# Optimization experiments

Hardware: AMD Instinct MI355X
Metric: run time of the kernel (lower is better)

## Reference

```python
import jax, jax.numpy as jnp
import numpy as np
from jax import lax

N, C_IN, C_OUT, H, W, K = 32, 512, 512, 56, 56, 7


def setup_inputs() -> dict:
    key = jax.random.key(0)
    ks = jax.random.split(key, 7)
    s_in = 1.0 / np.sqrt(C_IN)
    s_out = 1.0 / np.sqrt(C_OUT)
    return {
        "x": jax.random.normal(ks[0], (N, C_IN, H, W), dtype=jnp.float32),
        "k": K,
        "w_up": jax.random.normal(ks[1], (C_OUT, C_IN), dtype=jnp.float32) * s_in,
        "b_up": jax.random.normal(ks[2], (C_OUT,), dtype=jnp.float32) * s_in,
        "w_down": jax.random.normal(ks[3], (C_OUT, C_IN), dtype=jnp.float32) * s_in,
        "b_down": jax.random.normal(ks[4], (C_OUT,), dtype=jnp.float32) * s_in,
        "w_final": jax.random.normal(ks[5], (C_OUT, C_OUT), dtype=jnp.float32) * s_out,
        "b_final": jax.random.normal(ks[6], (C_OUT,), dtype=jnp.float32) * s_out,
    }


def _conv1x1(x, w, b):
    # x: [N, Cin, H, W], w: [Cout, Cin] -> [N, Cout, H, W]
    return jnp.einsum("nchw,oc->nohw", x, w) + b[None, :, None, None]


def reference(x, k, w_up, b_up, w_down, b_down, w_final, b_final):
    n, c_in, h, w = x.shape
    c_out = w_up.shape[0]
    pad = (k - 1) // 2

    up = _conv1x1(x, w_up, b_up)  # [N, Cout, H, W]

    # AdaptiveAvgPool2d(k): H, W divisible by k -> exact uniform pooling
    pooled = x.reshape(n, c_in, k, h // k, k, w // k).mean(axis=(3, 5))  # [N, Cin, k, k]
    down = _conv1x1(pooled, w_down, b_down)  # [N, Cout, k, k] dynamic depthwise kernels

    def dw_conv(u, ker):
        # u: [Cout, H, W], ker: [Cout, k, k]; depthwise (groups = Cout)
        return lax.conv_general_dilated(
            u[None],                    # [1, Cout, H, W]
            ker[:, None],               # [Cout, 1, k, k] (OIHW)
            window_strides=(1, 1),
            padding=[(pad, pad), (pad, pad)],
            feature_group_count=c_out,
            dimension_numbers=("NCHW", "OIHW", "NCHW"),
        )[0]

    out = jax.vmap(dw_conv)(up, down)  # [N, Cout, H, W]
    return _conv1x1(out, w_final, b_final)
```

## Files before the change

### kernel.cpp

```cpp
#include <hip/hip_runtime.h>
#include <hip/hip_bf16.h>

typedef unsigned short u16;
typedef _Float16 f16x8 __attribute__((ext_vector_type(8)));
typedef _Float16 f16x4 __attribute__((ext_vector_type(4)));
typedef _Float16 half2v __attribute__((ext_vector_type(2)));
typedef float f32x4 __attribute__((ext_vector_type(4)));
typedef unsigned short ushortx8 __attribute__((ext_vector_type(8)));
typedef unsigned short ushortx4 __attribute__((ext_vector_type(4)));

#define GPTR(p)  ((const __attribute__((address_space(1))) void*)(p))
#define LDSPTR(p) ((__attribute__((address_space(3))) void*)(p))

static __device__ __forceinline__ u16 f2h(float f) {
    _Float16 h = (_Float16)f;
    union { _Float16 h; u16 u; } v; v.h = h; return v.u;
}

__global__ __launch_bounds__(256) void cvtw_kernel(
    const float* __restrict__ wu, const float* __restrict__ wf,
    u16* __restrict__ wub, u16* __restrict__ wfb) {
    int i = blockIdx.x * 256 + threadIdx.x;
    wub[i] = f2h(wu[i]);
    wfb[i] = f2h(wf[i]);
}

__global__ __launch_bounds__(256) void transpose_kernel(
    const float* __restrict__ x, u16* __restrict__ xt) {
    __shared__ float tile[64][65];
    int bid = blockIdx.x;
    int jt = bid % 49;
    int r = bid / 49;
    int ct = r & 7, n = r >> 3;
    const float* src = x + ((size_t)(n * 512 + ct * 64)) * 3136 + jt * 64;
    for (int e = threadIdx.x; e < 1024; e += 256) {
        int i = e >> 4, j4 = (e & 15) * 4;
        float4 v = *(const float4*)(src + (size_t)i * 3136 + j4);
        tile[i][j4]     = v.x;
        tile[i][j4 + 1] = v.y;
        tile[i][j4 + 2] = v.z;
        tile[i][j4 + 3] = v.w;
    }
    __syncthreads();
    u16* dst = xt + ((size_t)(n * 3136 + jt * 64)) * 512 + ct * 64;
    for (int e = threadIdx.x; e < 1024; e += 256) {
        int jj = e >> 4, i4 = (e & 15) * 4;
        ushortx4 o;
        o[0] = f2h(tile[i4][jj]);
        o[1] = f2h(tile[i4 + 1][jj]);
        o[2] = f2h(tile[i4 + 2][jj]);
        o[3] = f2h(tile[i4 + 3][jj]);
        *(ushortx4*)(dst + (size_t)jj * 512 + i4) = o;
    }
}

__global__ __launch_bounds__(128) void poolh_kernel(
    const u16* __restrict__ xt, float* __restrict__ pooled) {
    int bid = blockIdx.x;
    int n = bid / 49, cell = bid - n * 49;
    int py = cell / 7, px = cell - py * 7;
    int t = threadIdx.x;
    float s0 = 0.f, s1 = 0.f, s2 = 0.f, s3 = 0.f;
    const u16* base = xt + ((size_t)(n * 3136 + py * 8 * 56 + px * 8)) * 512 + 4 * t;
    #pragma unroll
    for (int r = 0; r < 8; ++r) {
        #pragma unroll
        for (int cc = 0; cc < 8; ++cc) {
            f16x4 v = *(const f16x4*)(base + (size_t)(r * 56 + cc) * 512);
            s0 += (float)v[0]; s1 += (float)v[1];
            s2 += (float)v[2]; s3 += (float)v[3];
        }
    }
    float* pp = pooled + (size_t)n * 512 * 49 + py * 7 + px;
    pp[(size_t)(4 * t) * 49]     = s0 * (1.f / 64.f);
    pp[(size_t)(4 * t + 1) * 49] = s1 * (1.f / 64.f);
    pp[(size_t)(4 * t + 2) * 49] = s2 * (1.f / 64.f);
    pp[(size_t)(4 * t + 3) * 49] = s3 * (1.f / 64.f);
}

__global__ __launch_bounds__(256) void down_kernel(
    const float* __restrict__ pooled, const float* __restrict__ w_down,
    const float* __restrict__ b_down, float* __restrict__ down) {
    int bid = blockIdx.x;
    int n = bid >> 5, og = bid & 31;
    int wv = threadIdx.x >> 6, lane = threadIdx.x & 63;
    int o0 = og * 16 + wv * 4;
    const float* pp = pooled + (size_t)n * 512 * 49;
    const float* w0 = w_down + (size_t)o0 * 512;
    float a0 = 0, a1 = 0, a2 = 0, a3 = 0;
    int cell = lane < 49 ? lane : 48;
    #pragma unroll 4
    for (int c = 0; c < 512; ++c) {
        float p = pp[c * 49 + cell];
        a0 += p * w0[c];
        a1 += p * w0[512 + c];
        a2 += p * w0[1024 + c];
        a3 += p * w0[1536 + c];
    }
    if (lane < 49) {
        float* dd = down + ((size_t)n * 512 + o0) * 49 + lane;
        dd[0]   = a0 + b_down[o0];
        dd[49]  = a1 + b_down[o0 + 1];
        dd[98]  = a2 + b_down[o0 + 2];
        dd[147] = a3 + b_down[o0 + 3];
    }
}

template <int EPI>
__global__ __launch_bounds__(256) void gemm_kernel(
    const u16* __restrict__ A, const u16* __restrict__ Bt,
    const float* __restrict__ bias, void* __restrict__ Cout) {
    constexpr int K = 512;
    __shared__ u16 As[128 * 32];
    __shared__ u16 Bs[128 * 32];
    int tid = threadIdx.x, wv = tid >> 6, lane = tid & 63;
    int bid = blockIdx.x;
    int tm, tn;
    if (EPI == 0) { tm = (bid >> 5) * 8 + (bid & 7); tn = (bid >> 3) & 3; }
    else          { tn = (bid >> 5) * 8 + (bid & 7); tm = (bid >> 3) & 3; }
    size_t m0 = (size_t)tm * 128, n0 = (size_t)tn * 128;
    int lr = lane & 15, lk = (lane >> 4) * 8;
    int wr = wv >> 1, wc = wv & 1;

    int e0 = wv * 512 + lane * 8;
    int e1 = e0 + 2048;
    const u16* pa0 = A + (m0 + (size_t)(e0 >> 5)) * K + (e0 & 31);
    const u16* pa1 = A + (m0 + (size_t)(e1 >> 5)) * K + (e1 & 31);
    const u16* pb0 = Bt + (n0 + (size_t)(e0 >> 5)) * K + (e0 & 31);
    const u16* pb1 = Bt + (n0 + (size_t)(e1 >> 5)) * K + (e1 & 31);
    u16* sa0 = &As[wv * 512]; u16* sa1 = &As[wv * 512 + 2048];
    u16* sb0 = &Bs[wv * 512]; u16* sb1 = &Bs[wv * 512 + 2048];

    f32x4 acc[4][4] = {};

    for (int kt = 0; kt < K / 32; ++kt) {
        __builtin_amdgcn_global_load_lds(GPTR(pa0), LDSPTR(sa0), 16, 0, 0);
        __builtin_amdgcn_global_load_lds(GPTR(pa1), LDSPTR(sa1), 16, 0, 0);
        __builtin_amdgcn_global_load_lds(GPTR(pb0), LDSPTR(sb0), 16, 0, 0);
        __builtin_amdgcn_global_load_lds(GPTR(pb1), LDSPTR(sb1), 16, 0, 0);
        pa0 += 32; pa1 += 32; pb0 += 32; pb1 += 32;
        __syncthreads();
        f16x8 af[4], bfr[4];
        #pragma unroll
        for (int mi = 0; mi < 4; ++mi)
            af[mi] = *(const f16x8*)&As[(wr * 64 + mi * 16 + lr) * 32 + lk];
        #pragma unroll
        for (int ni = 0; ni < 4; ++ni)
            bfr[ni] = *(const f16x8*)&Bs[(wc * 64 + ni * 16 + lr) * 32 + lk];
        #pragma unroll
        for (int mi = 0; mi < 4; ++mi)
            #pragma unroll
            for (int ni = 0; ni < 4; ++ni)
                acc[mi][ni] = __builtin_amdgcn_mfma_f32_16x16x32_f16(af[mi], bfr[ni], acc[mi][ni], 0, 0, 0);
        __syncthreads();
    }

    if (EPI == 0) {
        u16* C = (u16*)Cout;
        #pragma unroll
        for (int ni = 0; ni < 4; ++ni) {
            size_t col = n0 + wc * 64 + ni * 16 + lr;
            float bv = bias[col];
            #pragma unroll
            for (int mi = 0; mi < 4; ++mi) {
                size_t rowb = m0 + wr * 64 + mi * 16 + (lane >> 4) * 4;
                ushortx4 pack;
                #pragma unroll
                for (int r = 0; r < 4; ++r)
                    pack[r] = f2h(acc[mi][ni][r] + bv);
                *(ushortx4*)&C[(rowb >> 3) * 4096 + col * 8 + (rowb & 7)] = pack;
            }
        }
    } else {
        float* C = (float*)Cout;
        #pragma unroll
        for (int ni = 0; ni < 4; ++ni) {
            int col = (int)(n0 + wc * 64 + ni * 16 + lr);
            int nimg = col / 3136;
            int jj = col - nimg * 3136;
            size_t obase = (size_t)nimg * 512 * 3136 + jj;
            #pragma unroll
            for (int mi = 0; mi < 4; ++mi) {
                int row = (int)(m0 + wr * 64 + mi * 16 + (lane >> 4) * 4);
                #pragma unroll
                for (int r = 0; r < 4; ++r)
                    C[obase + (size_t)(row + r) * 3136] = acc[mi][ni][r] + bias[row + r];
            }
        }
    }
}

__global__ __launch_bounds__(256) void dw_kernel(
    const u16* __restrict__ upb, const float* __restrict__ down,
    u16* __restrict__ dw) {
    __shared__ u16 tile[14 * 16 * 72];
    int bid = blockIdx.x;
    int n = bid / 224;
    int rem = bid - n * 224;
    int rt = rem >> 5;
    int cg = rem & 31;
    int tid = threadIdx.x;

    if (tid < 224)
        *(ushortx8*)&tile[tid * 72 + 56] = (ushortx8)0;

    for (int e = tid; e < 1568; e += 256) {
        int c = e & 15;
        int p = e >> 4;
        int hh = p / 7, jb = p - hh * 7;
        int h = rt * 8 + hh - 3;
        ushortx8 v = (ushortx8)0;
        if ((unsigned)h < 56u)
            v = *(const ushortx8*)(upb + ((size_t)(n * 392 + h * 7 + jb)) * 4096 + (cg * 16 + c) * 8);
        *(ushortx8*)&tile[(hh * 16 + c) * 72 + jb * 8] = v;
    }

    int c = tid & 15, u = tid >> 4;
    int row = u >> 1, wh = u & 1, w0 = wh * 28;
    const float* kp = down + ((size_t)n * 512 + cg * 16 + c) * 49;
    half2v kE[7][4], kO[7][4];
    #pragma unroll
    for (int ky = 0; ky < 7; ++ky) {
        float k0 = kp[ky*7+0], k1 = kp[ky*7+1], k2 = kp[ky*7+2], k3 = kp[ky*7+3];
        float k4 = kp[ky*7+4], k5 = kp[ky*7+5], k6 = kp[ky*7+6];
        kE[ky][0] = half2v{(_Float16)0.f, (_Float16)k0};
        kE[ky][1] = half2v{(_Float16)k1,  (_Float16)k2};
        kE[ky][2] = half2v{(_Float16)k3,  (_Float16)k4};
        kE[ky][3] = half2v{(_Float16)k5,  (_Float16)k6};
        kO[ky][0] = half2v{(_Float16)k0,  (_Float16)k1};
        kO[ky][1] = half2v{(_Float16)k2,  (_Float16)k3};
        kO[ky][2] = half2v{(_Float16)k4,  (_Float16)k5};
        kO[ky][3] = half2v{(_Float16)k6,  (_Float16)0.f};
    }
    __syncthreads();

    float acc[28];
    #pragma unroll
    for (int i = 0; i < 28; ++i) acc[i] = 0.f;

    #pragma unroll
    for (int ky = 0; ky < 7; ++ky) {
        const u16* rp = &tile[((row + ky) * 16 + c) * 72];
        half2v w2[18];
        #pragma unroll
        for (int t = 0; t < 9; ++t) {
            int p0 = ((w0 >> 1) - 2 + 2 * t) & 31;
            f16x4 q = *(const f16x4*)(rp + p0 * 2);
            w2[2*t]   = half2v{q[0], q[1]};
            w2[2*t+1] = half2v{q[2], q[3]};
        }
        #pragma unroll
        for (int m = 0; m < 14; ++m) {
            float ae = acc[2*m], ao = acc[2*m+1];
            ae = __builtin_amdgcn_fdot2(w2[m],   kE[ky][0], ae, false);
            ae = __builtin_amdgcn_fdot2(w2[m+1], kE[ky][1], ae, false);
            ae = __builtin_amdgcn_fdot2(w2[m+2], kE[ky][2], ae, false);
            ae = __builtin_amdgcn_fdot2(w2[m+3], kE[ky][3], ae, false);
            ao = __builtin_amdgcn_fdot2(w2[m+1], kO[ky][0], ao, false);
            ao = __builtin_amdgcn_fdot2(w2[m+2], kO[ky][1], ao, false);
            ao = __builtin_amdgcn_fdot2(w2[m+3], kO[ky][2], ao, false);
            ao = __builtin_amdgcn_fdot2(w2[m+4], kO[ky][3], ao, false);
            acc[2*m] = ae; acc[2*m+1] = ao;
        }
    }

    int h = rt * 8 + row;
    u16* op = dw + ((size_t)(n * 3136 + h * 56 + w0)) * 512 + cg * 16 + c;
    #pragma unroll
    for (int i = 0; i < 28; ++i)
        op[(size_t)i * 512] = f2h(acc[i]);
}

extern "C" void kernel_launch(void* const* d_in, const int* in_sizes, int n_in,
                              void* d_out, int out_size, void* d_ws, size_t ws_size,
                              hipStream_t stream) {
    const float* x       = (const float*)d_in[0];
    const float* w_up    = (const float*)d_in[2];
    const float* b_up    = (const float*)d_in[3];
    const float* w_down  = (const float*)d_in[4];
    const float* b_down  = (const float*)d_in[5];
    const float* w_final = (const float*)d_in[6];
    const float* b_final = (const float*)d_in[7];

    char* ws = (char*)d_ws;
    u16*   xt     = (u16*)  (ws + 0);
    u16*   upb    = (u16*)  (ws + 102760448);
    float* pooled = (float*)(ws + 205520896);
    float* down   = (float*)(ws + 208732160);
    u16*   wub    = (u16*)  (ws + 211943424);
    u16*   wfb    = (u16*)  (ws + 212467712);
    u16*   dwb    = xt;

    cvtw_kernel<<<1024, 256, 0, stream>>>(w_up, w_final, wub, wfb);
    transpose_kernel<<<12544, 256, 0, stream>>>(x, xt);
    poolh_kernel<<<1568, 128, 0, stream>>>(xt, pooled);
    down_kernel<<<1024, 256, 0, stream>>>(pooled, w_down, b_down, down);
    gemm_kernel<0><<<3136, 256, 0, stream>>>(xt, wub, b_up, upb);
    dw_kernel<<<7168, 256, 0, stream>>>(upb, down, dwb);
    gemm_kernel<1><<<3136, 256, 0, stream>>>(wfb, dwb, b_final, d_out);
}
```

Before: 412.6 us.

## Load streaming GEMM operand directly to registers and double-buffer the shared one in LDS

The GEMM kernel used to stage both A and B tiles through LDS each k-step. Now the operand unique to each block (the large-dimension side) is read straight from global into registers and prefetched one k-step ahead. The shared 128-row operand is double-buffered in LDS via global_load_lds, with explicit vmcnt waits and raw barriers. This halves LDS traffic and overlaps the next tile's loads with MFMA work, but it relies on hand-counted vmcnt values and uses uncoalesced direct global fragment loads.

```diff
diff --git a/kernel.cpp b/kernel.cpp
--- a/kernel.cpp
+++ b/kernel.cpp
@@ -111,48 +111,71 @@
     const u16* __restrict__ A, const u16* __restrict__ Bt,
     const float* __restrict__ bias, void* __restrict__ Cout) {
     constexpr int K = 512;
-    __shared__ u16 As[128 * 32];
-    __shared__ u16 Bs[128 * 32];
+    constexpr int NT = 16;
+    __shared__ u16 Rs[2][4096];
     int tid = threadIdx.x, wv = tid >> 6, lane = tid & 63;
     int bid = blockIdx.x;
-    int tm, tn;
-    if (EPI == 0) { tm = (bid >> 5) * 8 + (bid & 7); tn = (bid >> 3) & 3; }
-    else          { tn = (bid >> 5) * 8 + (bid & 7); tm = (bid >> 3) & 3; }
-    size_t m0 = (size_t)tm * 128, n0 = (size_t)tn * 128;
+    int sbig = (bid >> 5) * 8 + (bid & 7);
+    int sres = (bid >> 3) & 3;
+    size_t s0 = (size_t)sbig * 128;
+    size_t r0 = (size_t)sres * 128;
+    size_t m0 = EPI == 0 ? s0 : r0;
+    size_t n0 = EPI == 0 ? r0 : s0;
+    const u16* Sp = EPI == 0 ? A : Bt;
+    const u16* Rp = EPI == 0 ? Bt : A;
+
     int lr = lane & 15, lk = (lane >> 4) * 8;
     int wr = wv >> 1, wc = wv & 1;
+    int wsel = EPI == 0 ? wr : wc;
+    int wres = EPI == 0 ? wc : wr;
+
+    const u16* sbase = Sp + (s0 + (size_t)(wsel * 64) + lr) * K + lk;
 
     int e0 = wv * 512 + lane * 8;
-    int e1 = e0 + 2048;
-    const u16* pa0 = A + (m0 + (size_t)(e0 >> 5)) * K + (e0 & 31);
-    const u16* pa1 = A + (m0 + (size_t)(e1 >> 5)) * K + (e1 & 31);
-    const u16* pb0 = Bt + (n0 + (size_t)(e0 >> 5)) * K + (e0 & 31);
-    const u16* pb1 = Bt + (n0 + (size_t)(e1 >> 5)) * K + (e1 & 31);
-    u16* sa0 = &As[wv * 512]; u16* sa1 = &As[wv * 512 + 2048];
-    u16* sb0 = &Bs[wv * 512]; u16* sb1 = &Bs[wv * 512 + 2048];
+    const u16* pr0 = Rp + (r0 + (size_t)(e0 >> 5)) * K + (e0 & 31);
+    const u16* pr1 = Rp + (r0 + (size_t)((e0 + 2048) >> 5)) * K + (e0 & 31);
 
     f32x4 acc[4][4] = {};
-
-    for (int kt = 0; kt < K / 32; ++kt) {
-        __builtin_amdgcn_global_load_lds(GPTR(pa0), LDSPTR(sa0), 16, 0, 0);
-        __builtin_amdgcn_global_load_lds(GPTR(pa1), LDSPTR(sa1), 16, 0, 0);
-        __builtin_amdgcn_global_load_lds(GPTR(pb0), LDSPTR(sb0), 16, 0, 0);
-        __builtin_amdgcn_global_load_lds(GPTR(pb1), LDSPTR(sb1), 16, 0, 0);
-        pa0 += 32; pa1 += 32; pb0 += 32; pb1 += 32;
-        __syncthreads();
-        f16x8 af[4], bfr[4];
+    f16x8 sc[4], sn[4];
+
+    __builtin_amdgcn_global_load_lds(GPTR(pr0), LDSPTR(&Rs[0][wv * 512]), 16, 0, 0);
+    __builtin_amdgcn_global_load_lds(GPTR(pr1), LDSPTR(&Rs[0][wv * 512 + 2048]), 16, 0, 0);
+    #pragma unroll
+    for (int i = 0; i < 4; ++i)
+        sc[i] = *(const f16x8*)(sbase + (size_t)i * 16 * K);
+
+    for (int kt = 0; kt < NT; ++kt) {
+        if (kt + 1 < NT) {
+            #pragma unroll
+            for (int i = 0; i < 4; ++i)
+                sn[i] = *(const f16x8*)(sbase + (size_t)i * 16 * K + (kt + 1) * 32);
+            int b = (kt + 1) & 1;
+            __builtin_amdgcn_global_load_lds(GPTR(pr0 + (kt + 1) * 32), LDSPTR(&Rs[b][wv * 512]), 16, 0, 0);
+            __builtin_amdgcn_global_load_lds(GPTR(pr1 + (kt + 1) * 32), LDSPTR(&Rs[b][wv * 512 + 2048]), 16, 0, 0);
+            asm volatile("s_waitcnt vmcnt(6)" ::: "memory");
+        } else {
+            asm volatile("s_waitcnt vmcnt(0)" ::: "memory");
+        }
+        __builtin_amdgcn_s_barrier();
+        f16x8 rf[4];
+        #pragma unroll
+        for (int i = 0; i < 4; ++i)
+            rf[i] = *(const f16x8*)&Rs[kt & 1][(wres * 64 + i * 16 + lr) * 32 + lk];
         #pragma unroll
         for (int mi = 0; mi < 4; ++mi)
-            af[mi] = *(const f16x8*)&As[(wr * 64 + mi * 16 + lr) * 32 + lk];
-        #pragma unroll
-        for (int ni = 0; ni < 4; ++ni)
-            bfr[ni] = *(const f16x8*)&Bs[(wc * 64 + ni * 16 + lr) * 32 + lk];
-        #pragma unroll
-        for (int mi = 0; mi < 4; ++mi)
-            #pragma unroll
-            for (int ni = 0; ni < 4; ++ni)
-                acc[mi][ni] = __builtin_amdgcn_mfma_f32_16x16x32_f16(af[mi], bfr[ni], acc[mi][ni], 0, 0, 0);
-        __syncthreads();
+            #pragma unroll
+            for (int ni = 0; ni < 4; ++ni) {
+                if (EPI == 0)
+                    acc[mi][ni] = __builtin_amdgcn_mfma_f32_16x16x32_f16(sc[mi], rf[ni], acc[mi][ni], 0, 0, 0);
+                else
+                    acc[mi][ni] = __builtin_amdgcn_mfma_f32_16x16x32_f16(rf[mi], sc[ni], acc[mi][ni], 0, 0, 0);
+            }
+        asm volatile("s_waitcnt lgkmcnt(0)" ::: "memory");
+        __builtin_amdgcn_s_barrier();
+        if (kt + 1 < NT) {
+            #pragma unroll
+            for (int i = 0; i < 4; ++i) sc[i] = sn[i];
+        }
     }
 
     if (EPI == 0) {
```

Result: slower. 501.3 us (+21.5%).

## Use single-wave 64x64 GEMM blocks with double-buffered LDS prefetch

Applied to the files above, without the earlier changes.

Both 1x1-conv GEMMs move from 256-thread blocks computing 128x128 tiles to single-wavefront blocks computing 64x64 tiles. LDS is double-buffered, and the next K-slice is prefetched with global_load_lds before computing on the current one. Explicit waitcnt instructions replace __syncthreads, since one wave needs no barrier. This targets barrier stalls and load latency, but it halves operand reuse per block, so global and L2 traffic rise.

```diff
diff --git a/kernel.cpp b/kernel.cpp
--- a/kernel.cpp
+++ b/kernel.cpp
@@ -107,63 +107,71 @@
 }
 
 template <int EPI>
-__global__ __launch_bounds__(256) void gemm_kernel(
+__global__ __launch_bounds__(64) void gemm_kernel(
     const u16* __restrict__ A, const u16* __restrict__ Bt,
     const float* __restrict__ bias, void* __restrict__ Cout) {
-    constexpr int K = 512;
-    __shared__ u16 As[128 * 32];
-    __shared__ u16 Bs[128 * 32];
-    int tid = threadIdx.x, wv = tid >> 6, lane = tid & 63;
-    int bid = blockIdx.x;
-    int tm, tn;
-    if (EPI == 0) { tm = (bid >> 5) * 8 + (bid & 7); tn = (bid >> 3) & 3; }
-    else          { tn = (bid >> 5) * 8 + (bid & 7); tm = (bid >> 3) & 3; }
-    size_t m0 = (size_t)tm * 128, n0 = (size_t)tn * 128;
-    int lr = lane & 15, lk = (lane >> 4) * 8;
-    int wr = wv >> 1, wc = wv & 1;
-
-    int e0 = wv * 512 + lane * 8;
-    int e1 = e0 + 2048;
-    const u16* pa0 = A + (m0 + (size_t)(e0 >> 5)) * K + (e0 & 31);
-    const u16* pa1 = A + (m0 + (size_t)(e1 >> 5)) * K + (e1 & 31);
-    const u16* pb0 = Bt + (n0 + (size_t)(e0 >> 5)) * K + (e0 & 31);
-    const u16* pb1 = Bt + (n0 + (size_t)(e1 >> 5)) * K + (e1 & 31);
-    u16* sa0 = &As[wv * 512]; u16* sa1 = &As[wv * 512 + 2048];
-    u16* sb0 = &Bs[wv * 512]; u16* sb1 = &Bs[wv * 512 + 2048];
+    constexpr int NT = 16;
+    __shared__ u16 As[2][2048];
+    __shared__ u16 Bs[2][2048];
+    int l = threadIdx.x;
+    int lr = l & 15, lk = (l >> 4) * 8;
+    int d = blockIdx.x;
+    int big = d % 1568, res = d / 1568;
+    size_t m0, n0;
+    if (EPI == 0) { m0 = (size_t)big * 64; n0 = (size_t)res * 64; }
+    else          { m0 = (size_t)res * 64; n0 = (size_t)big * 64; }
+
+    int srow = l >> 2, scol = (l & 3) * 8;
+    const u16* pa = A  + (m0 + (size_t)srow) * 512 + scol;
+    const u16* pb = Bt + (n0 + (size_t)srow) * 512 + scol;
 
     f32x4 acc[4][4] = {};
 
-    for (int kt = 0; kt < K / 32; ++kt) {
-        __builtin_amdgcn_global_load_lds(GPTR(pa0), LDSPTR(sa0), 16, 0, 0);
-        __builtin_amdgcn_global_load_lds(GPTR(pa1), LDSPTR(sa1), 16, 0, 0);
-        __builtin_amdgcn_global_load_lds(GPTR(pb0), LDSPTR(sb0), 16, 0, 0);
-        __builtin_amdgcn_global_load_lds(GPTR(pb1), LDSPTR(sb1), 16, 0, 0);
-        pa0 += 32; pa1 += 32; pb0 += 32; pb1 += 32;
-        __syncthreads();
+#define STAGE1(bf, kt) do { \
+    __builtin_amdgcn_global_load_lds(GPTR(pa + (size_t)( 0) * 512 + (kt) * 32), LDSPTR(&As[bf][0]),    16, 0, 0); \
+    __builtin_amdgcn_global_load_lds(GPTR(pb + (size_t)( 0) * 512 + (kt) * 32), LDSPTR(&Bs[bf][0]),    16, 0, 0); \
+    __builtin_amdgcn_global_load_lds(GPTR(pa + (size_t)(16) * 512 + (kt) * 32), LDSPTR(&As[bf][512]),  16, 0, 0); \
+    __builtin_amdgcn_global_load_lds(GPTR(pb + (size_t)(16) * 512 + (kt) * 32), LDSPTR(&Bs[bf][512]),  16, 0, 0); \
+    __builtin_amdgcn_global_load_lds(GPTR(pa + (size_t)(32) * 512 + (kt) * 32), LDSPTR(&As[bf][1024]), 16, 0, 0); \
+    __builtin_amdgcn_global_load_lds(GPTR(pb + (size_t)(32) * 512 + (kt) * 32), LDSPTR(&Bs[bf][1024]), 16, 0, 0); \
+    __builtin_amdgcn_global_load_lds(GPTR(pa + (size_t)(48) * 512 + (kt) * 32), LDSPTR(&As[bf][1536]), 16, 0, 0); \
+    __builtin_amdgcn_global_load_lds(GPTR(pb + (size_t)(48) * 512 + (kt) * 32), LDSPTR(&Bs[bf][1536]), 16, 0, 0); \
+  } while (0)
+
+    STAGE1(0, 0);
+    for (int kt = 0; kt < NT; ++kt) {
+        int cur = kt & 1;
+        if (kt + 1 < NT) {
+            asm volatile("s_waitcnt lgkmcnt(0)" ::: "memory");
+            STAGE1(cur ^ 1, kt + 1);
+            asm volatile("s_waitcnt vmcnt(8)" ::: "memory");
+        } else {
+            asm volatile("s_waitcnt vmcnt(0)" ::: "memory");
+        }
         f16x8 af[4], bfr[4];
         #pragma unroll
         for (int mi = 0; mi < 4; ++mi)
-            af[mi] = *(const f16x8*)&As[(wr * 64 + mi * 16 + lr) * 32 + lk];
+            af[mi] = *(const f16x8*)&As[cur][(mi * 16 + lr) * 32 + lk];
         #pragma unroll
         for (int ni = 0; ni < 4; ++ni)
-            bfr[ni] = *(const f16x8*)&Bs[(wc * 64 + ni * 16 + lr) * 32 + lk];
+            bfr[ni] = *(const f16x8*)&Bs[cur][(ni * 16 + lr) * 32 + lk];
         #pragma unroll
         for (int mi = 0; mi < 4; ++mi)
             #pragma unroll
             for (int ni = 0; ni < 4; ++ni)
                 acc[mi][ni] = __builtin_amdgcn_mfma_f32_16x16x32_f16(af[mi], bfr[ni], acc[mi][ni], 0, 0, 0);
-        __syncthreads();
-    }
+    }
+#undef STAGE1
 
     if (EPI == 0) {
         u16* C = (u16*)Cout;
         #pragma unroll
         for (int ni = 0; ni < 4; ++ni) {
-            size_t col = n0 + wc * 64 + ni * 16 + lr;
+            size_t col = n0 + ni * 16 + lr;
             float bv = bias[col];
             #pragma unroll
             for (int mi = 0; mi < 4; ++mi) {
-                size_t rowb = m0 + wr * 64 + mi * 16 + (lane >> 4) * 4;
+                size_t rowb = m0 + mi * 16 + (l >> 4) * 4;
                 ushortx4 pack;
                 #pragma unroll
                 for (int r = 0; r < 4; ++r)
@@ -175,13 +183,13 @@
         float* C = (float*)Cout;
         #pragma unroll
         for (int ni = 0; ni < 4; ++ni) {
-            int col = (int)(n0 + wc * 64 + ni * 16 + lr);
+            int col = (int)(n0 + ni * 16 + lr);
             int nimg = col / 3136;
             int jj = col - nimg * 3136;
             size_t obase = (size_t)nimg * 512 * 3136 + jj;
             #pragma unroll
             for (int mi = 0; mi < 4; ++mi) {
-                int row = (int)(m0 + wr * 64 + mi * 16 + (lane >> 4) * 4);
+                int row = (int)(m0 + mi * 16 + (l >> 4) * 4);
                 #pragma unroll
                 for (int r = 0; r < 4; ++r)
                     C[obase + (size_t)(row + r) * 3136] = acc[mi][ni][r] + bias[row + r];
@@ -295,7 +303,7 @@
     transpose_kernel<<<12544, 256, 0, stream>>>(x, xt);
     poolh_kernel<<<1568, 128, 0, stream>>>(xt, pooled);
     down_kernel<<<1024, 256, 0, stream>>>(pooled, w_down, b_down, down);
-    gemm_kernel<0><<<3136, 256, 0, stream>>>(xt, wub, b_up, upb);
+    gemm_kernel<0><<<12544, 64, 0, stream>>>(xt, wub, b_up, upb);
     dw_kernel<<<7168, 256, 0, stream>>>(upb, down, dwb);
-    gemm_kernel<1><<<3136, 256, 0, stream>>>(wfb, dwb, b_final, d_out);
-}
+    gemm_kernel<1><<<12544, 64, 0, stream>>>(wfb, dwb, b_final, d_out);
+}
```

Measured after the change: 536.8 us. +30.1%, slower.
